# Kernel tuning notes

Hardware: AMD Instinct MI355X
Metric: run time of the kernel (lower is better)

## Reference

```python
import jax, jax.numpy as jnp
import numpy as np

N, E, F_IN, D, L = 100000, 1600000, 32, 128, 5
B, V, T, EMB = 3000, 64, 128, 64
H = L * D  # 640 LSTM hidden
BN_EPS = 1e-5


def setup_inputs():
    key = jax.random.key(0)
    ks = jax.random.split(key, 20)
    rn = lambda k, s, sc=0.05: jax.random.normal(k, s, jnp.float32) * sc
    inp = {
        'x': jax.random.normal(ks[0], (N, F_IN), jnp.float32),
        'edge_index': jax.random.randint(ks[1], (2, E), 0, N, jnp.int32),
        'batch': jnp.sort(jax.random.randint(ks[2], (N,), 0, B, jnp.int32)),
        'smi': jax.random.randint(ks[3], (B, T), 0, V, jnp.int32),
        'gin0_w1': rn(ks[4], (F_IN, D)), 'gin0_b1': jnp.zeros((D,), jnp.float32),
        'gin0_w2': rn(ks[5], (D, D)),    'gin0_b2': jnp.zeros((D,), jnp.float32),
        'ginr_w1': rn(ks[6], (L - 1, D, D)), 'ginr_b1': jnp.zeros((L - 1, D), jnp.float32),
        'ginr_w2': rn(ks[7], (L - 1, D, D)), 'ginr_b2': jnp.zeros((L - 1, D), jnp.float32),
        'bn_gamma': jnp.ones((L, D), jnp.float32), 'bn_beta': jnp.zeros((L, D), jnp.float32),
        'emb': rn(ks[8], (V, EMB), 0.1).at[0].set(0.0),  # padding_idx=0
        'w_ih': rn(ks[9], (4 * H, EMB), 0.04), 'w_hh': rn(ks[10], (4 * H, H), 0.04),
        'b_ih': jnp.zeros((4 * H,), jnp.float32), 'b_hh': jnp.zeros((4 * H,), jnp.float32),
        'g_w1': rn(ks[11], (L * D, 4 * D)), 'g_b1': jnp.zeros((4 * D,), jnp.float32),
        'g_bn_gamma': jnp.ones((4 * D,), jnp.float32), 'g_bn_beta': jnp.zeros((4 * D,), jnp.float32),
        'g_w2': rn(ks[12], (4 * D, 6 * D)),
    }
    return inp


def _bn(h, gamma, beta):
    # BatchNorm1d in training mode: biased batch statistics
    mu = h.mean(0)
    var = h.var(0)
    return (h - mu) * jax.lax.rsqrt(var + BN_EPS) * gamma + beta


def _gin_layer(h, src, dst, w1, b1, w2, b2, gamma, beta):
    # GINConv (eps=0): MLP(x + sum_{j->i} x_j), then ReLU, then BN
    agg = jax.ops.segment_sum(h[src], dst, num_segments=N)  # [N, d]
    z = h + agg
    z = jnp.maximum(z @ w1 + b1, 0.0) @ w2 + b2
    z = jnp.maximum(z, 0.0)
    return _bn(z, gamma, beta)


def _lstm_last(e, w_ih, w_hh, b_ih, b_hh):
    # e: [B, T, EMB] -> last hidden state [B, H]
    def step(carry, xt):
        h, c = carry
        gates = xt @ w_ih.T + b_ih + h @ w_hh.T + b_hh  # [B, 4H]
        i, f, g, o = jnp.split(gates, 4, axis=1)  # torch gate order i,f,g,o
        c = jax.nn.sigmoid(f) * c + jax.nn.sigmoid(i) * jnp.tanh(g)
        h = jax.nn.sigmoid(o) * jnp.tanh(c)
        return (h, c), None
    h0 = jnp.zeros((e.shape[0], H), e.dtype)
    (h, _), _ = jax.lax.scan(step, (h0, h0), e.transpose(1, 0, 2))
    return h


def reference(x, edge_index, batch, smi, gin0_w1, gin0_b1, gin0_w2, gin0_b2,
              ginr_w1, ginr_b1, ginr_w2, ginr_b2, bn_gamma, bn_beta, emb,
              w_ih, w_hh, b_ih, b_hh, g_w1, g_b1, g_bn_gamma, g_bn_beta, g_w2):
    src, dst = edge_index[0], edge_index[1]
    # --- GIN encoder with layer-wise global_add_pool ---
    h = _gin_layer(x, src, dst, gin0_w1, gin0_b1, gin0_w2, gin0_b2, bn_gamma[0], bn_beta[0])
    pools = [jax.ops.segment_sum(h, batch, num_segments=B)]
    for i in range(L - 1):
        h = _gin_layer(h, src, dst, ginr_w1[i], ginr_b1[i], ginr_w2[i], ginr_b2[i],
                       bn_gamma[i + 1], bn_beta[i + 1])
        pools.append(jax.ops.segment_sum(h, batch, num_segments=B))
    enc1 = jnp.concatenate(pools, axis=1)  # [B, L*D]
    # --- SMILES encoder: Embedding + LSTM, take output at last timestep ---
    enc2 = _lstm_last(emb[smi], w_ih, w_hh, b_ih, b_hh)  # [B, H] == [B, L*D]
    # --- shared projection head g, L2-normalized (F.normalize, eps=1e-12) ---
    def g_head(z):
        z1 = jnp.maximum(_bn(z @ g_w1 + g_b1, g_bn_gamma, g_bn_beta), 0.0)
        out = z1 @ g_w2
        nrm = jnp.maximum(jnp.linalg.norm(out, axis=1, keepdims=True), 1e-12)
        return out / nrm
    return (g_head(enc1), g_head(enc2))
```

## Files before the change

### kernel.cpp

```cpp
#include <hip/hip_runtime.h>

typedef __bf16 bf16x8 __attribute__((ext_vector_type(8)));
typedef float f32x4 __attribute__((ext_vector_type(4)));
typedef unsigned short ushort8 __attribute__((ext_vector_type(8)));

#define DEV static __device__ __forceinline__

DEV unsigned short f2bf(float f){
  unsigned int u = __builtin_bit_cast(unsigned int, f);
  u += 0x7fffu + ((u >> 16) & 1u);
  return (unsigned short)(u >> 16);
}
DEV float bf2f(unsigned short u){
  return __builtin_bit_cast(float, ((unsigned int)u) << 16);
}
DEV float bfu_lo(unsigned int v){ return __builtin_bit_cast(float, v << 16); }
DEV float bfu_hi(unsigned int v){ return __builtin_bit_cast(float, v & 0xFFFF0000u); }
DEV float sigf(float x){ return 1.0f/(1.0f + __expf(-x)); }
DEV float tanhf_fast(float x){
  float ax = fabsf(x);
  float e = __expf(2.0f*ax);
  float r = 1.0f - 2.0f/(e + 1.0f);
  return copysignf(r, x);
}

static constexpr int NN   = 100000;
static constexpr int NPAD = 100096;
static constexpr int NE   = 1600000;
static constexpr int NB   = 3000;
static constexpr int BPAD = 3072;
static constexpr int TT   = 128;
static constexpr int HID  = 640;
static constexpr int SCAN_B = 1024;
static constexpr int NBLK = (NN + SCAN_B - 1)/SCAN_B;

__global__ void cvt_k(const float* __restrict__ s, unsigned short* __restrict__ d, int n){
  int i = blockIdx.x*256 + threadIdx.x; if (i < n) d[i] = f2bf(s[i]);
}
__global__ void transpose_cvt_split_k(const float* __restrict__ s, unsigned short* __restrict__ dh,
                                      unsigned short* __restrict__ dl, int R, int C){
  int i = blockIdx.x*256 + threadIdx.x; if (i >= R*C) return;
  int r = i / C, c = i - r*C;
  float v = s[i];
  unsigned short hi = f2bf(v);
  dh[c*R + r] = hi;
  dl[c*R + r] = f2bf(v - bf2f(hi));
}
__global__ void wc2_build_k(const float* __restrict__ whh, const float* __restrict__ wih,
                            unsigned short* __restrict__ wc2){
  int i = blockIdx.x*256 + threadIdx.x; if (i >= 2560*704) return;
  int n2 = i / 704, k = i - n2*704;
  int jt = n2 >> 7, rem = n2 & 127;
  int hc = rem >> 6, gate = (rem >> 4) & 3, j15 = rem & 15;
  int n = gate*640 + jt*32 + hc*16 + j15;
  float v = (k < 640) ? whh[n*640 + k] : wih[n*64 + (k - 640)];
  wc2[i] = f2bf(v);
}
__global__ void add_k(const float* __restrict__ a, const float* __restrict__ b, float* __restrict__ o, int n){
  int i = blockIdx.x*256 + threadIdx.x; if (i < n) o[i] = a[i] + b[i];
}

__global__ __launch_bounds__(256) void deg_hist_k(const int* __restrict__ dsts, int* __restrict__ deg){
  int e = blockIdx.x*256 + threadIdx.x; if (e < NE) atomicAdd(&deg[dsts[e]], 1);
}
__global__ __launch_bounds__(256) void scan_bsum_k(const int* __restrict__ deg, int* __restrict__ bsum){
  __shared__ int red[4];
  int b = blockIdx.x, tid = threadIdx.x;
  int base = b*SCAN_B + tid*4;
  int s = 0;
  #pragma unroll
  for (int q = 0; q < 4; ++q){ int idx = base + q; s += (idx < NN) ? deg[idx] : 0; }
  #pragma unroll
  for (int m = 1; m < 64; m <<= 1) s += __shfl_xor(s, m);
  if ((tid & 63) == 0) red[tid >> 6] = s;
  __syncthreads();
  if (tid == 0) bsum[b] = red[0] + red[1] + red[2] + red[3];
}
__global__ void scan_off_k(int* __restrict__ bsum){
  if (threadIdx.x == 0){
    int run = 0;
    for (int i = 0; i < NBLK; ++i){ int t = bsum[i]; bsum[i] = run; run += t; }
  }
}
__global__ __launch_bounds__(256) void scan_write_k(const int* __restrict__ deg, const int* __restrict__ bsum,
                                                    int* __restrict__ rowptr, int* __restrict__ cursor){
  __shared__ int tsum[256];
  int b = blockIdx.x, tid = threadIdx.x;
  int base = b*SCAN_B + tid*4;
  int v[4]; int s = 0;
  #pragma unroll
  for (int q = 0; q < 4; ++q){ int idx = base + q; v[q] = (idx < NN) ? deg[idx] : 0; s += v[q]; }
  tsum[tid] = s;
  __syncthreads();
  for (int offt = 1; offt < 256; offt <<= 1){
    int y = (tid >= offt) ? tsum[tid - offt] : 0;
    __syncthreads();
    tsum[tid] += y;
    __syncthreads();
  }
  int run = bsum[b] + tsum[tid] - s;
  #pragma unroll
  for (int q = 0; q < 4; ++q){
    int idx = base + q;
    if (idx < NN){ rowptr[idx] = run; cursor[idx] = run; }
    run += v[q];
  }
  if (b == 0 && tid == 0) rowptr[NN] = NE;
}
__global__ __launch_bounds__(256) void csr_fill_k(const int* __restrict__ srcs, const int* __restrict__ dsts,
                                                  int* __restrict__ cursor, int* __restrict__ eidx){
  int e = blockIdx.x*256 + threadIdx.x; if (e >= NE) return;
  int d = dsts[e];
  int pos = atomicAdd(&cursor[d], 1);
  eidx[pos] = srcs[e];
}

__global__ __launch_bounds__(256) void gbound_k(const int* __restrict__ batch, int* __restrict__ gstart){
  int i = blockIdx.x*256 + threadIdx.x;
  if (i >= NN) return;
  int bi = batch[i];
  int bp = (i == 0) ? -1 : batch[i-1];
  for (int g = bp + 1; g <= bi; ++g) gstart[g] = i;
  if (i == NN-1){
    for (int g = bi + 1; g <= NB; ++g) gstart[g] = NN;
  }
}

__global__ __launch_bounds__(256) void agg128_k(const int* __restrict__ rowptr, const int* __restrict__ eidx,
    const unsigned int* __restrict__ Hbf, float* __restrict__ Z){
  int wid = (blockIdx.x*256 + threadIdx.x) >> 6;
  if (wid >= NN) return;
  int lane = threadIdx.x & 63;
  int n0 = rowptr[wid], n1 = rowptr[wid+1];
  unsigned int v = Hbf[(size_t)wid*64 + lane];
  float ax = bfu_lo(v), ay = bfu_hi(v);
  int i = n0;
  for (; i + 1 < n1; i += 2){
    int s0 = eidx[i], s1 = eidx[i+1];
    unsigned int v0 = Hbf[(size_t)s0*64 + lane];
    unsigned int v1 = Hbf[(size_t)s1*64 + lane];
    ax += bfu_lo(v0) + bfu_lo(v1);
    ay += bfu_hi(v0) + bfu_hi(v1);
  }
  if (i < n1){
    unsigned int v0 = Hbf[(size_t)eidx[i]*64 + lane];
    ax += bfu_lo(v0); ay += bfu_hi(v0);
  }
  ((float2*)Z)[(size_t)wid*64 + lane] = make_float2(ax, ay);
}
__global__ __launch_bounds__(256) void agg32_k(const int* __restrict__ rowptr, const int* __restrict__ eidx,
    const float* __restrict__ X, float* __restrict__ Z){
  int r = (blockIdx.x*256 + threadIdx.x) >> 5;
  if (r >= NN) return;
  int l = threadIdx.x & 31;
  int n0 = rowptr[r], n1 = rowptr[r+1];
  float acc = X[(size_t)r*32 + l];
  int i = n0;
  for (; i + 1 < n1; i += 2){
    int s0 = eidx[i], s1 = eidx[i+1];
    acc += X[(size_t)s0*32 + l] + X[(size_t)s1*32 + l];
  }
  if (i < n1) acc += X[(size_t)eidx[i]*32 + l];
  Z[(size_t)r*32 + l] = acc;
}

template<int KIN>
__global__ __launch_bounds__(256) void gin_mlp_k(const float* __restrict__ Z,
    const unsigned short* __restrict__ W1h, const unsigned short* __restrict__ W1l,
    const unsigned short* __restrict__ W2h, const unsigned short* __restrict__ W2l,
    const float* __restrict__ b1, const float* __restrict__ b2,
    float* __restrict__ Y, float* __restrict__ stats)
{
  constexpr int SA = KIN + 8;
  __shared__ __align__(16) unsigned short Ah[128*136];
  __shared__ __align__(16) unsigned short Al[128*136];
  const int tid = threadIdx.x, lane = tid & 63, w = tid >> 6;
  const int row0 = blockIdx.x * 128;
  const int wr = (w >> 1)*64, wc0 = (w & 1)*64;
  const int l15 = lane & 15, lg = lane >> 4;

  constexpr int CH = KIN/8;
  #pragma unroll
  for (int i = 0; i < (128*CH)/256; ++i){
    int chunk = tid + 256*i;
    int row = chunk / CH, kc = (chunk - row*CH)*8;
    const float* sp = Z + (size_t)(row0 + row)*KIN + kc;
    float4 a0 = *(const float4*)sp;
    float4 a1 = *(const float4*)(sp + 4);
    float vv[8] = {a0.x,a0.y,a0.z,a0.w,a1.x,a1.y,a1.z,a1.w};
    ushort8 vh, vl;
    #pragma unroll
    for (int q=0;q<8;++q){ unsigned short h = f2bf(vv[q]); vh[q]=h; vl[q]=f2bf(vv[q]-bf2f(h)); }
    *(ushort8*)&Ah[row*SA + kc] = vh;
    *(ushort8*)&Al[row*SA + kc] = vl;
  }
  __syncthreads();

  f32x4 acc[4][4];
  #pragma unroll
  for (int i=0;i<4;++i)
    #pragma unroll
    for (int j=0;j<4;++j) acc[i][j] = (f32x4)(0.0f);

  #pragma unroll
  for (int k0 = 0; k0 < KIN; k0 += 32){
    bf16x8 ah[4], al[4], bh[4], bl[4];
    #pragma unroll
    for (int fa=0; fa<4; ++fa){
      ah[fa] = *(const bf16x8*)&Ah[(wr + fa*16 + l15)*SA + k0 + 8*lg];
      al[fa] = *(const bf16x8*)&Al[(wr + fa*16 + l15)*SA + k0 + 8*lg];
    }
    #pragma unroll
    for (int fb=0; fb<4; ++fb){
      bh[fb] = *(const bf16x8*)&W1h[(wc0 + fb*16 + l15)*KIN + k0 + 8*lg];
      bl[fb] = *(const bf16x8*)&W1l[(wc0 + fb*16 + l15)*KIN + k0 + 8*lg];
    }
    #pragma unroll
    for (int fa=0; fa<4; ++fa)
      #pragma unroll
      for (int fb=0; fb<4; ++fb){
        acc[fa][fb] = __builtin_amdgcn_mfma_f32_16x16x32_bf16(ah[fa], bh[fb], acc[fa][fb], 0, 0, 0);
        acc[fa][fb] = __builtin_amdgcn_mfma_f32_16x16x32_bf16(al[fa], bh[fb], acc[fa][fb], 0, 0, 0);
        acc[fa][fb] = __builtin_amdgcn_mfma_f32_16x16x32_bf16(ah[fa], bl[fb], acc[fa][fb], 0, 0, 0);
      }
  }
  __syncthreads();

  {
    float b1v[4];
    #pragma unroll
    for (int fb=0; fb<4; ++fb) b1v[fb] = b1[wc0 + fb*16 + l15];
    #pragma unroll
    for (int fa=0; fa<4; ++fa)
      #pragma unroll
      for (int fb=0; fb<4; ++fb)
        #pragma unroll
        for (int r=0; r<4; ++r){
          float v = fmaxf(acc[fa][fb][r] + b1v[fb], 0.0f);
          unsigned short h = f2bf(v);
          int idx = (wr + fa*16 + lg*4 + r)*136 + (wc0 + fb*16 + l15);
          Ah[idx] = h;
          Al[idx] = f2bf(v - bf2f(h));
        }
  }
  __syncthreads();

  f32x4 acc2[4][4];
  #pragma unroll
  for (int i=0;i<4;++i)
    #pragma unroll
    for (int j=0;j<4;++j) acc2[i][j] = (f32x4)(0.0f);

  #pragma unroll
  for (int k0 = 0; k0 < 128; k0 += 32){
    bf16x8 ah[4], al[4], bh[4], bl[4];
    #pragma unroll
    for (int fa=0; fa<4; ++fa){
      ah[fa] = *(const bf16x8*)&Ah[(wr + fa*16 + l15)*136 + k0 + 8*lg];
      al[fa] = *(const bf16x8*)&Al[(wr + fa*16 + l15)*136 + k0 + 8*lg];
    }
    #pragma unroll
    for (int fb=0; fb<4; ++fb){
      bh[fb] = *(const bf16x8*)&W2h[(wc0 + fb*16 + l15)*128 + k0 + 8*lg];
      bl[fb] = *(const bf16x8*)&W2l[(wc0 + fb*16 + l15)*128 + k0 + 8*lg];
    }
    #pragma unroll
    for (int fa=0; fa<4; ++fa)
      #pragma unroll
      for (int fb=0; fb<4; ++fb){
        acc2[fa][fb] = __builtin_amdgcn_mfma_f32_16x16x32_bf16(ah[fa], bh[fb], acc2[fa][fb], 0, 0, 0);
        acc2[fa][fb] = __builtin_amdgcn_mfma_f32_16x16x32_bf16(al[fa], bh[fb], acc2[fa][fb], 0, 0, 0);
        acc2[fa][fb] = __builtin_amdgcn_mfma_f32_16x16x32_bf16(ah[fa], bl[fb], acc2[fa][fb], 0, 0, 0);
      }
  }

  float b2v[4]; int cc[4];
  #pragma unroll
  for (int fb=0; fb<4; ++fb){ cc[fb] = wc0 + fb*16 + l15; b2v[fb] = b2[cc[fb]]; }
  float ps[4] = {0,0,0,0}, pq[4] = {0,0,0,0};
  #pragma unroll
  for (int fa=0; fa<4; ++fa)
    #pragma unroll
    for (int fb=0; fb<4; ++fb)
      #pragma unroll
      for (int r=0; r<4; ++r){
        int row = row0 + wr + fa*16 + lg*4 + r;
        float v = fmaxf(acc2[fa][fb][r] + b2v[fb], 0.0f);
        if (row < NN){
          Y[(size_t)row*128 + cc[fb]] = v;
          ps[fb] += v; pq[fb] += v*v;
        }
      }
  #pragma unroll
  for (int fb=0; fb<4; ++fb){
    float s = ps[fb]; s += __shfl_xor(s, 16); s += __shfl_xor(s, 32);
    float q = pq[fb]; q += __shfl_xor(q, 16); q += __shfl_xor(q, 32);
    if (lane < 16){ atomicAdd(&stats[cc[fb]], s); atomicAdd(&stats[128 + cc[fb]], q); }
  }
}

__global__ void bn_finalize_k(const float* __restrict__ stats, const float* __restrict__ gamma,
                              const float* __restrict__ beta, float* __restrict__ sshift, int C, float invN){
  int c = blockIdx.x*blockDim.x + threadIdx.x; if (c >= C) return;
  float mean = stats[c]*invN;
  float var  = fmaxf(stats[C+c]*invN - mean*mean, 0.0f);
  float inv  = rsqrtf(var + 1e-5f);
  float sc   = gamma[c]*inv;
  sshift[c] = sc; sshift[C+c] = beta[c] - mean*sc;
}

__global__ __launch_bounds__(256) void bn_pool_k(const float* __restrict__ Y,
    const float* __restrict__ sshift, const int* __restrict__ gstart,
    unsigned int* __restrict__ Hbf, float* __restrict__ pool, int layer)
{
  int g = blockIdx.x*4 + (threadIdx.x >> 6);
  if (g >= NB) return;
  int lane = threadIdx.x & 63;
  int c0 = lane << 1;
  float sc0 = sshift[c0],     sc1 = sshift[c0+1];
  float sh0 = sshift[128+c0], sh1 = sshift[128+c0+1];
  int n0 = gstart[g], n1 = gstart[g+1];
  const float2* Yp = (const float2*)Y;
  float2 acc = make_float2(0.f, 0.f);
  for (int r = n0; r < n1; ++r){
    float2 y = Yp[(size_t)r*64 + lane];
    float hx = y.x*sc0 + sh0;
    float hy = y.y*sc1 + sh1;
    Hbf[(size_t)r*64 + lane] = (unsigned int)f2bf(hx) | ((unsigned int)f2bf(hy) << 16);
    acc.x += hx; acc.y += hy;
  }
  ((float2*)pool)[(size_t)g*320 + layer*64 + lane] = acc;
}

__global__ __launch_bounds__(256) void embed_k(const int* __restrict__ smi,
    const unsigned short* __restrict__ emb_bf, unsigned short* __restrict__ e2){
  int gid = blockIdx.x*256 + threadIdx.x;
  int tb = gid >> 4;
  if (tb >= TT*BPAD) return;
  int t = tb / BPAD, b = tb - t*BPAD;
  int k4 = (gid & 15) << 2;
  uint2 v = make_uint2(0u, 0u);
  if (b < NB){
    int tok = smi[b*TT + t];
    v = *(const uint2*)&emb_bf[tok*64 + k4];
  }
  *(uint2*)&e2[(size_t)tb*64 + k4] = v;
}

__global__ __launch_bounds__(256) void lstm_step_k(const unsigned short* __restrict__ hprev,
    unsigned short* __restrict__ hnext, float* __restrict__ cbuf,
    const unsigned short* __restrict__ e2, const unsigned short* __restrict__ Wc2,
    const float* __restrict__ biasc, int t, float* __restrict__ hfin)
{
  __shared__ __align__(16) unsigned short As[2][128*40];
  __shared__ __align__(16) unsigned short Bs[2][128*40];
  const int tid = threadIdx.x, lane = tid & 63, w = tid >> 6;
  const int bid = blockIdx.x;
  const int xcd = bid & 7, idx = bid >> 3;
  const int rt = xcd*3 + (idx % 3);
  const int jt = idx / 3;
  const int row0 = rt * 128;
  const int l15 = lane & 15, lg = lane >> 4;
  const int wr = (w >> 1)*64, wc0 = (w & 1)*64;

  const int srow = tid >> 2, skc = (tid & 3) << 3;
  const unsigned short* A0 = hprev + (size_t)(row0 + srow)*HID;
  const unsigned short* A1 = hprev + (size_t)(row0 + srow + 64)*HID;
  const unsigned short* E0 = e2 + ((size_t)t*BPAD + row0 + srow)*64;
  const unsigned short* E1 = e2 + ((size_t)t*BPAD + row0 + srow + 64)*64;
  const unsigned short* B0 = Wc2 + (size_t)(jt*128 + srow)*704;
  const unsigned short* B1 = Wc2 + (size_t)(jt*128 + srow + 64)*704;

  *(ushort8*)&As[0][srow*40 + skc]      = *(const ushort8*)&A0[skc];
  *(ushort8*)&As[0][(srow+64)*40 + skc] = *(const ushort8*)&A1[skc];
  *(ushort8*)&Bs[0][srow*40 + skc]      = *(const ushort8*)&B0[skc];
  *(ushort8*)&Bs[0][(srow+64)*40 + skc] = *(const ushort8*)&B1[skc];
  __syncthreads();

  f32x4 acc[4][4];
  #pragma unroll
  for (int i=0;i<4;++i)
    #pragma unroll
    for (int j=0;j<4;++j) acc[i][j] = (f32x4)(0.0f);

  int p = 0;
  for (int kk = 0; kk < 22; ++kk){
    ushort8 va0, va1, vb0, vb1;
    const int k1 = (kk+1)*32;
    if (kk < 21){
      if (k1 < 640){
        va0 = *(const ushort8*)&A0[k1 + skc];
        va1 = *(const ushort8*)&A1[k1 + skc];
      } else {
        va0 = *(const ushort8*)&E0[k1 - 640 + skc];
        va1 = *(const ushort8*)&E1[k1 - 640 + skc];
      }
      vb0 = *(const ushort8*)&B0[k1 + skc];
      vb1 = *(const ushort8*)&B1[k1 + skc];
    }
    bf16x8 a[4], b[4];
    #pragma unroll
    for (int fa=0; fa<4; ++fa) a[fa] = *(const bf16x8*)&As[p][(wr + fa*16 + l15)*40 + 8*lg];
    #pragma unroll
    for (int fb=0; fb<4; ++fb) b[fb] = *(const bf16x8*)&Bs[p][(wc0 + fb*16 + l15)*40 + 8*lg];
    __builtin_amdgcn_s_setprio(1);
    #pragma unroll
    for (int fa=0; fa<4; ++fa)
      #pragma unroll
      for (int fb=0; fb<4; ++fb)
        acc[fa][fb] = __builtin_amdgcn_mfma_f32_16x16x32_bf16(a[fa], b[fb], acc[fa][fb], 0, 0, 0);
    __builtin_amdgcn_s_setprio(0);
    if (kk < 21){
      *(ushort8*)&As[p^1][srow*40 + skc]      = va0;
      *(ushort8*)&As[p^1][(srow+64)*40 + skc] = va1;
      *(ushort8*)&Bs[p^1][srow*40 + skc]      = vb0;
      *(ushort8*)&Bs[p^1][(srow+64)*40 + skc] = vb1;
    }
    __syncthreads();
    p ^= 1;
  }

  const int j = jt*32 + (w & 1)*16 + l15;
  float bi = biasc[j], bf_ = biasc[640+j], bg = biasc[1280+j], bo = biasc[1920+j];
  #pragma unroll
  for (int fa=0; fa<4; ++fa){
    #pragma unroll
    for (int r=0; r<4; ++r){
      int br = row0 + wr + fa*16 + lg*4 + r;
      float iv = acc[fa][0][r] + bi;
      float fv = acc[fa][1][r] + bf_;
      float gv = acc[fa][2][r] + bg;
      float ov = acc[fa][3][r] + bo;
      size_t idx2 = (size_t)br*HID + j;
      float co = cbuf[idx2];
      float cn = sigf(fv)*co + sigf(iv)*tanhf_fast(gv);
      cbuf[idx2] = cn;
      float hv = sigf(ov)*tanhf_fast(cn);
      hnext[idx2] = f2bf(hv);
      if (hfin) hfin[idx2] = hv;
    }
  }
}

template<int DO_STATS>
__global__ __launch_bounds__(256) void gemm_split_k(const float* __restrict__ A,
    const unsigned short* __restrict__ Bh, const unsigned short* __restrict__ Bl,
    const float* __restrict__ bias, float* __restrict__ outp, float* __restrict__ stats,
    int Mvalid, int Nc, int K)
{
  __shared__ __align__(16) unsigned short Ah[128*40];
  __shared__ __align__(16) unsigned short Al[128*40];
  const int tid = threadIdx.x, lane = tid & 63, w = tid >> 6;
  const int row0 = blockIdx.x * 128, col0 = blockIdx.y * 128;
  const int wr = (w >> 1)*64, wc0 = (w & 1)*64;
  const int l15 = lane & 15, lg = lane >> 4;

  f32x4 acc[4][4];
  #pragma unroll
  for (int i=0;i<4;++i)
    #pragma unroll
    for (int j=0;j<4;++j) acc[i][j] = (f32x4)(0.0f);

  for (int k0 = 0; k0 < K; k0 += 32){
    #pragma unroll
    for (int i=0;i<2;++i){
      int chunk = tid + 256*i;
      int row = chunk >> 2, kc = (chunk & 3) << 3;
      const float* sp = A + (size_t)(row0+row)*K + k0 + kc;
      float4 a0 = *(const float4*)sp;
      float4 a1 = *(const float4*)(sp + 4);
      float vv[8] = {a0.x,a0.y,a0.z,a0.w,a1.x,a1.y,a1.z,a1.w};
      ushort8 vh, vl;
      #pragma unroll
      for (int q=0;q<8;++q){ unsigned short h = f2bf(vv[q]); vh[q]=h; vl[q]=f2bf(vv[q]-bf2f(h)); }
      *(ushort8*)&Ah[row*40 + kc] = vh;
      *(ushort8*)&Al[row*40 + kc] = vl;
    }
    __syncthreads();
    bf16x8 ah[4], al[4], bh[4], bl[4];
    #pragma unroll
    for (int fa=0; fa<4; ++fa){
      ah[fa] = *(const bf16x8*)&Ah[(wr + fa*16 + l15)*40 + 8*lg];
      al[fa] = *(const bf16x8*)&Al[(wr + fa*16 + l15)*40 + 8*lg];
    }
    #pragma unroll
    for (int fb=0; fb<4; ++fb){
      bh[fb] = *(const bf16x8*)&Bh[(size_t)(col0 + wc0 + fb*16 + l15)*K + k0 + 8*lg];
      bl[fb] = *(const bf16x8*)&Bl[(size_t)(col0 + wc0 + fb*16 + l15)*K + k0 + 8*lg];
    }
    #pragma unroll
    for (int fa=0; fa<4; ++fa)
      #pragma unroll
      for (int fb=0; fb<4; ++fb){
        acc[fa][fb] = __builtin_amdgcn_mfma_f32_16x16x32_bf16(ah[fa], bh[fb], acc[fa][fb], 0, 0, 0);
        acc[fa][fb] = __builtin_amdgcn_mfma_f32_16x16x32_bf16(al[fa], bh[fb], acc[fa][fb], 0, 0, 0);
        acc[fa][fb] = __builtin_amdgcn_mfma_f32_16x16x32_bf16(ah[fa], bl[fb], acc[fa][fb], 0, 0, 0);
      }
    __syncthreads();
  }

  float bv[4]; int cc[4];
  #pragma unroll
  for (int fb=0; fb<4; ++fb){ cc[fb] = col0 + wc0 + fb*16 + l15; bv[fb] = bias ? bias[cc[fb]] : 0.0f; }
  float ps[4] = {0,0,0,0}, pq[4] = {0,0,0,0};
  #pragma unroll
  for (int fa=0; fa<4; ++fa)
    #pragma unroll
    for (int fb=0; fb<4; ++fb)
      #pragma unroll
      for (int r=0; r<4; ++r){
        int row = row0 + wr + fa*16 + lg*4 + r;
        float v = acc[fa][fb][r] + bv[fb];
        if (row < Mvalid){
          outp[(size_t)row*Nc + cc[fb]] = v;
          if (DO_STATS){ ps[fb] += v; pq[fb] += v*v; }
        }
      }
  if (DO_STATS){
    #pragma unroll
    for (int fb=0; fb<4; ++fb){
      float s = ps[fb]; s += __shfl_xor(s, 16); s += __shfl_xor(s, 32);
      float q = pq[fb]; q += __shfl_xor(q, 16); q += __shfl_xor(q, 32);
      if (lane < 16){ atomicAdd(&stats[cc[fb]], s); atomicAdd(&stats[Nc + cc[fb]], q); }
    }
  }
}

__global__ __launch_bounds__(256) void bn_apply_head_k(const float* __restrict__ Zpre,
    const float* __restrict__ sshift, float* __restrict__ z1f){
  int gid = blockIdx.x*256 + threadIdx.x;
  int r = gid >> 7;
  if (r >= BPAD) return;
  int c0 = (gid & 127) << 2;
  float4 o = make_float4(0.f,0.f,0.f,0.f);
  if (r < NB){
    float4 v = *(const float4*)&Zpre[(size_t)r*512 + c0];
    o.x = fmaxf(v.x*sshift[c0+0] + sshift[512+c0+0], 0.0f);
    o.y = fmaxf(v.y*sshift[c0+1] + sshift[512+c0+1], 0.0f);
    o.z = fmaxf(v.z*sshift[c0+2] + sshift[512+c0+2], 0.0f);
    o.w = fmaxf(v.w*sshift[c0+3] + sshift[512+c0+3], 0.0f);
  }
  *(float4*)&z1f[(size_t)r*512 + c0] = o;
}

__global__ __launch_bounds__(256) void rownorm_k(const float* __restrict__ in, float* __restrict__ outp){
  int r = blockIdx.x;
  const float* p = in + (size_t)r*768;
  float ss = 0.0f;
  #pragma unroll
  for (int i = 0; i < 3; ++i){ float v = p[threadIdx.x + 256*i]; ss += v*v; }
  #pragma unroll
  for (int m = 1; m < 64; m <<= 1) ss += __shfl_xor(ss, m);
  __shared__ float red[4];
  if ((threadIdx.x & 63) == 0) red[threadIdx.x >> 6] = ss;
  __syncthreads();
  float tot = red[0] + red[1] + red[2] + red[3];
  float inv = 1.0f / fmaxf(sqrtf(tot), 1e-12f);
  float* q = outp + (size_t)r*768;
  #pragma unroll
  for (int i = 0; i < 3; ++i) q[threadIdx.x + 256*i] = p[threadIdx.x + 256*i]*inv;
}

static inline int cdiv(long a, long b){ return (int)((a + b - 1)/b); }

extern "C" void kernel_launch(void* const* d_in, const int* in_sizes, int n_in,
                              void* d_out, int out_size, void* d_ws, size_t ws_size,
                              hipStream_t stream)
{
  const float* x        = (const float*)d_in[0];
  const int*   edges    = (const int*)d_in[1];
  const int*   batch    = (const int*)d_in[2];
  const int*   smi      = (const int*)d_in[3];
  const float* gin0_w1  = (const float*)d_in[4];
  const float* gin0_b1  = (const float*)d_in[5];
  const float* gin0_w2  = (const float*)d_in[6];
  const float* gin0_b2  = (const float*)d_in[7];
  const float* ginr_w1  = (const float*)d_in[8];
  const float* ginr_b1  = (const float*)d_in[9];
  const float* ginr_w2  = (const float*)d_in[10];
  const float* ginr_b2  = (const float*)d_in[11];
  const float* bn_gamma = (const float*)d_in[12];
  const float* bn_beta  = (const float*)d_in[13];
  const float* emb      = (const float*)d_in[14];
  const float* w_ih     = (const float*)d_in[15];
  const float* w_hh     = (const float*)d_in[16];
  const float* b_ih     = (const float*)d_in[17];
  const float* b_hh     = (const float*)d_in[18];
  const float* g_w1     = (const float*)d_in[19];
  const float* g_b1     = (const float*)d_in[20];
  const float* g_bng    = (const float*)d_in[21];
  const float* g_bnb    = (const float*)d_in[22];
  const float* g_w2     = (const float*)d_in[23];
  float* outp = (float*)d_out;
  const int* srcs = edges;
  const int* dsts = edges + NE;

  char* base = (char*)d_ws;
  size_t off = 0;
  auto carve = [&](size_t bytes)->char*{ char* p = base + off; off += (bytes + 255) & ~(size_t)255; return p; };
  float* z_gin = (float*)carve((size_t)NPAD*128*4);
  float* y_gin = (float*)carve((size_t)NPAD*128*4);
  float* h_gin = (float*)carve((size_t)NPAD*128*4);
  float* pool  = (float*)carve((size_t)BPAD*HID*4);
  unsigned short* Wc2    = (unsigned short*)carve((size_t)2560*704*2);
  float*          biasc  = (float*)carve(2560*4);
  unsigned short* emb_bf = (unsigned short*)carve(4096*2);
  unsigned short* w1t0h  = (unsigned short*)carve(128*32*2);
  unsigned short* w1t0l  = (unsigned short*)carve(128*32*2);
  unsigned short* w2t0h  = (unsigned short*)carve(128*128*2);
  unsigned short* w2t0l  = (unsigned short*)carve(128*128*2);
  unsigned short* w1trh  = (unsigned short*)carve(4*16384*2);
  unsigned short* w1trl  = (unsigned short*)carve(4*16384*2);
  unsigned short* w2trh  = (unsigned short*)carve(4*16384*2);
  unsigned short* w2trl  = (unsigned short*)carve(4*16384*2);
  unsigned short* gw1th  = (unsigned short*)carve(512*640*2);
  unsigned short* gw1tl  = (unsigned short*)carve(512*640*2);
  unsigned short* gw2th  = (unsigned short*)carve(768*512*2);
  unsigned short* gw2tl  = (unsigned short*)carve(768*512*2);
  float* stats  = (float*)carve(1024*4);
  float* sshift = (float*)carve(1024*4);
  int* deg    = (int*)carve((size_t)NN*4);
  int* cursor = (int*)carve((size_t)NN*4);
  int* rowptr = (int*)carve((size_t)(NN+1)*4);
  int* bsum   = (int*)carve(512);
  int* eidx   = (int*)carve((size_t)NE*4);
  int* gstart = (int*)carve((size_t)(NB+1)*4);

  unsigned int*   h_bf   = (unsigned int*)h_gin;
  unsigned short* e2     = (unsigned short*)y_gin;
  unsigned short* h_a    = (unsigned short*)h_gin;
  unsigned short* h_b    = h_a + (size_t)BPAD*HID;
  float*          c_buf  = (float*)(h_b + (size_t)BPAD*HID);
  float*          hfin   = c_buf + (size_t)BPAD*HID;
  float*          z1pre  = (float*)z_gin;
  float*          z1f    = z1pre + (size_t)BPAD*512;
  float*          outtmp = z1f + (size_t)BPAD*512;

  wc2_build_k<<<cdiv((long)2560*704,256),256,0,stream>>>(w_hh, w_ih, Wc2);
  add_k<<<cdiv(2560,256),256,0,stream>>>(b_ih, b_hh, biasc, 2560);
  cvt_k<<<cdiv(4096,256),256,0,stream>>>(emb, emb_bf, 4096);
  transpose_cvt_split_k<<<cdiv(32*128,256),256,0,stream>>>(gin0_w1, w1t0h, w1t0l, 32, 128);
  transpose_cvt_split_k<<<cdiv(16384,256),256,0,stream>>>(gin0_w2, w2t0h, w2t0l, 128, 128);
  for (int i = 0; i < 4; ++i){
    transpose_cvt_split_k<<<cdiv(16384,256),256,0,stream>>>(ginr_w1 + (size_t)i*16384, w1trh + (size_t)i*16384, w1trl + (size_t)i*16384, 128, 128);
    transpose_cvt_split_k<<<cdiv(16384,256),256,0,stream>>>(ginr_w2 + (size_t)i*16384, w2trh + (size_t)i*16384, w2trl + (size_t)i*16384, 128, 128);
  }
  transpose_cvt_split_k<<<cdiv(640*512,256),256,0,stream>>>(g_w1, gw1th, gw1tl, 640, 512);
  transpose_cvt_split_k<<<cdiv(512*768,256),256,0,stream>>>(g_w2, gw2th, gw2tl, 512, 768);

  hipMemsetAsync(deg, 0, (size_t)NN*4, stream);
  deg_hist_k<<<cdiv(NE,256),256,0,stream>>>(dsts, deg);
  scan_bsum_k<<<NBLK,256,0,stream>>>(deg, bsum);
  scan_off_k<<<1,64,0,stream>>>(bsum);
  scan_write_k<<<NBLK,256,0,stream>>>(deg, bsum, rowptr, cursor);
  csr_fill_k<<<cdiv(NE,256),256,0,stream>>>(srcs, dsts, cursor, eidx);
  gbound_k<<<cdiv(NN,256),256,0,stream>>>(batch, gstart);

  for (int l = 0; l < 5; ++l){
    hipMemsetAsync(stats, 0, 1024*4, stream);
    if (l == 0)
      agg32_k<<<cdiv((long)NN*32,256),256,0,stream>>>(rowptr, eidx, x, z_gin);
    else
      agg128_k<<<cdiv((long)NN*64,256),256,0,stream>>>(rowptr, eidx, h_bf, z_gin);
    if (l == 0)
      gin_mlp_k<32><<<NPAD/128,256,0,stream>>>(z_gin, w1t0h, w1t0l, w2t0h, w2t0l, gin0_b1, gin0_b2, y_gin, stats);
    else
      gin_mlp_k<128><<<NPAD/128,256,0,stream>>>(z_gin, w1trh + (size_t)(l-1)*16384, w1trl + (size_t)(l-1)*16384,
                                                w2trh + (size_t)(l-1)*16384, w2trl + (size_t)(l-1)*16384,
                                                ginr_b1 + (l-1)*128, ginr_b2 + (l-1)*128, y_gin, stats);
    bn_finalize_k<<<1,128,0,stream>>>(stats, bn_gamma + l*128, bn_beta + l*128, sshift, 128, 1.0f/NN);
    bn_pool_k<<<cdiv(NB,4),256,0,stream>>>(y_gin, sshift, gstart, h_bf, pool, l);
  }

  embed_k<<<cdiv((long)TT*BPAD*16,256),256,0,stream>>>(smi, emb_bf, e2);
  hipMemsetAsync(h_a, 0, (size_t)BPAD*HID*2, stream);
  hipMemsetAsync(c_buf, 0, (size_t)BPAD*HID*4, stream);
  for (int t = 0; t < TT; ++t){
    const unsigned short* hin = (t & 1) ? h_b : h_a;
    unsigned short* hout      = (t & 1) ? h_a : h_b;
    lstm_step_k<<<480,256,0,stream>>>(hin, hout, c_buf, e2, Wc2, biasc, t,
                                      (t == TT-1) ? hfin : nullptr);
  }

  const float* headAf[2] = { pool, hfin };
  for (int hd = 0; hd < 2; ++hd){
    hipMemsetAsync(stats, 0, 1024*4, stream);
    gemm_split_k<1><<<dim3(BPAD/128, 4),256,0,stream>>>(headAf[hd], gw1th, gw1tl, g_b1, z1pre, stats, NB, 512, 640);
    bn_finalize_k<<<2,256,0,stream>>>(stats, g_bng, g_bnb, sshift, 512, 1.0f/NB);
    bn_apply_head_k<<<cdiv((long)BPAD*128,256),256,0,stream>>>(z1pre, sshift, z1f);
    gemm_split_k<0><<<dim3(BPAD/128, 6),256,0,stream>>>(z1f, gw2th, gw2tl, nullptr, outtmp, nullptr, NB, 768, 512);
    rownorm_k<<<NB,256,0,stream>>>(outtmp, outp + (size_t)hd*NB*768);
  }
}
```

Before: 4.282 ms.

## Load LSTM step MFMA operands directly from global memory instead of LDS

The LSTM step kernel no longer stages the hidden-state and weight tiles through double-buffered shared memory with barriers. Each wave now loads its MFMA fragments straight from global memory, and the K loop is fully unrolled. This removes LDS traffic and __syncthreads, at the cost of more redundant global and L2 reads, since both waves sharing a row or column fetch the same data, and the loads are less coalesced.

```diff
diff --git a/kernel.cpp b/kernel.cpp
--- a/kernel.cpp
+++ b/kernel.cpp
@@ -352,8 +352,6 @@
     const unsigned short* __restrict__ e2, const unsigned short* __restrict__ Wc2,
     const float* __restrict__ biasc, int t, float* __restrict__ hfin)
 {
-  __shared__ __align__(16) unsigned short As[2][128*40];
-  __shared__ __align__(16) unsigned short Bs[2][128*40];
   const int tid = threadIdx.x, lane = tid & 63, w = tid >> 6;
   const int bid = blockIdx.x;
   const int xcd = bid & 7, idx = bid >> 3;
@@ -363,19 +361,17 @@
   const int l15 = lane & 15, lg = lane >> 4;
   const int wr = (w >> 1)*64, wc0 = (w & 1)*64;
 
-  const int srow = tid >> 2, skc = (tid & 3) << 3;
-  const unsigned short* A0 = hprev + (size_t)(row0 + srow)*HID;
-  const unsigned short* A1 = hprev + (size_t)(row0 + srow + 64)*HID;
-  const unsigned short* E0 = e2 + ((size_t)t*BPAD + row0 + srow)*64;
-  const unsigned short* E1 = e2 + ((size_t)t*BPAD + row0 + srow + 64)*64;
-  const unsigned short* B0 = Wc2 + (size_t)(jt*128 + srow)*704;
-  const unsigned short* B1 = Wc2 + (size_t)(jt*128 + srow + 64)*704;
-
-  *(ushort8*)&As[0][srow*40 + skc]      = *(const ushort8*)&A0[skc];
-  *(ushort8*)&As[0][(srow+64)*40 + skc] = *(const ushort8*)&A1[skc];
-  *(ushort8*)&Bs[0][srow*40 + skc]      = *(const ushort8*)&B0[skc];
-  *(ushort8*)&Bs[0][(srow+64)*40 + skc] = *(const ushort8*)&B1[skc];
-  __syncthreads();
+  const unsigned short* Ab[4];
+  const unsigned short* Eb[4];
+  const unsigned short* Bb[4];
+  #pragma unroll
+  for (int fa=0; fa<4; ++fa){
+    Ab[fa] = hprev + (size_t)(row0 + wr + fa*16 + l15)*HID + 8*lg;
+    Eb[fa] = e2 + ((size_t)t*BPAD + row0 + wr + fa*16 + l15)*64 + 8*lg;
+  }
+  #pragma unroll
+  for (int fb=0; fb<4; ++fb)
+    Bb[fb] = Wc2 + (size_t)(jt*128 + wc0 + fb*16 + l15)*704 + 8*lg;
 
   f32x4 acc[4][4];
   #pragma unroll
@@ -383,41 +379,22 @@
     #pragma unroll
     for (int j=0;j<4;++j) acc[i][j] = (f32x4)(0.0f);
 
-  int p = 0;
+  #pragma unroll
   for (int kk = 0; kk < 22; ++kk){
-    ushort8 va0, va1, vb0, vb1;
-    const int k1 = (kk+1)*32;
-    if (kk < 21){
-      if (k1 < 640){
-        va0 = *(const ushort8*)&A0[k1 + skc];
-        va1 = *(const ushort8*)&A1[k1 + skc];
-      } else {
-        va0 = *(const ushort8*)&E0[k1 - 640 + skc];
-        va1 = *(const ushort8*)&E1[k1 - 640 + skc];
-      }
-      vb0 = *(const ushort8*)&B0[k1 + skc];
-      vb1 = *(const ushort8*)&B1[k1 + skc];
-    }
+    const int k0 = kk*32;
     bf16x8 a[4], b[4];
     #pragma unroll
-    for (int fa=0; fa<4; ++fa) a[fa] = *(const bf16x8*)&As[p][(wr + fa*16 + l15)*40 + 8*lg];
-    #pragma unroll
-    for (int fb=0; fb<4; ++fb) b[fb] = *(const bf16x8*)&Bs[p][(wc0 + fb*16 + l15)*40 + 8*lg];
-    __builtin_amdgcn_s_setprio(1);
+    for (int fa=0; fa<4; ++fa)
+      a[fa] = (k0 < 640) ? *(const bf16x8*)(Ab[fa] + k0)
+                         : *(const bf16x8*)(Eb[fa] + (k0 - 640));
+    #pragma unroll
+    for (int fb=0; fb<4; ++fb)
+      b[fb] = *(const bf16x8*)(Bb[fb] + k0);
     #pragma unroll
     for (int fa=0; fa<4; ++fa)
       #pragma unroll
       for (int fb=0; fb<4; ++fb)
         acc[fa][fb] = __builtin_amdgcn_mfma_f32_16x16x32_bf16(a[fa], b[fb], acc[fa][fb], 0, 0, 0);
-    __builtin_amdgcn_s_setprio(0);
-    if (kk < 21){
-      *(ushort8*)&As[p^1][srow*40 + skc]      = va0;
-      *(ushort8*)&As[p^1][(srow+64)*40 + skc] = va1;
-      *(ushort8*)&Bs[p^1][srow*40 + skc]      = vb0;
-      *(ushort8*)&Bs[p^1][(srow+64)*40 + skc] = vb1;
-    }
-    __syncthreads();
-    p ^= 1;
   }
 
   const int j = jt*32 + (w & 1)*16 + l15;
```

Result: slower. 7.425 ms (+73.4%).
